# Optimization experiments

Measured on AMD Instinct MI355X. Metric: run time of the kernel, lower is better.

Reference implementation:

```python
import jax, jax.numpy as jnp
import numpy as np


def gin_layer(x, src, dst, ew, w1, b1, w2, b2):
    # message: gather source features, scale by edge weight  [E, d]
    msg = x[src] * ew[:, None]
    # scatter-add into destination nodes  [N, d]
    agg = jax.ops.segment_sum(msg, dst, num_segments=x.shape[0])
    # GIN update: (1 + eps) * x + aggregate, eps = 0 (default)
    h = agg + x
    # 2-layer MLP (Linear -> ReLU -> Linear, plain last layer)
    h = jax.nn.relu(h @ w1 + b1)
    return h @ w2 + b2


def setup_inputs() -> dict:
    key = jax.random.key(0)
    ks = jax.random.split(key, 16)
    N, E, D = 100000, 1000000, 64
    x = jax.random.normal(ks[0], (N, D), dtype=jnp.float32)
    edge_index = jax.random.randint(ks[1], (2, E), 0, N)
    edge_weight = jax.random.uniform(ks[2], (E,), dtype=jnp.float32)

    def lin(k, fi, fo):
        return jax.random.normal(k, (fi, fo), dtype=jnp.float32) * (1.0 / np.sqrt(fi))

    return {
        "x": x, "edge_index": edge_index, "edge_weight": edge_weight,
        "w11": lin(ks[3], 64, 64),  "b11": jnp.zeros(64, jnp.float32),
        "w12": lin(ks[4], 64, 64),  "b12": jnp.zeros(64, jnp.float32),
        "w21": lin(ks[5], 64, 128), "b21": jnp.zeros(128, jnp.float32),
        "w22": lin(ks[6], 128, 64), "b22": jnp.zeros(64, jnp.float32),
        "w31": lin(ks[7], 64, 64),  "b31": jnp.zeros(64, jnp.float32),
        "w32": lin(ks[8], 64, 64),  "b32": jnp.zeros(64, jnp.float32),
    }


def reference(x, edge_index, edge_weight,
              w11, b11, w12, b12,
              w21, b21, w22, b22,
              w31, b31, w32, b32):
    src, dst = edge_index[0], edge_index[1]
    # dropout is identity in eval mode
    h = gin_layer(x, src, dst, edge_weight, w11, b11, w12, b12)
    h = jax.nn.relu(h)
    h = gin_layer(h, src, dst, edge_weight, w21, b21, w22, b22)
    h = jax.nn.relu(h)
    h = gin_layer(h, src, dst, edge_weight, w31, b31, w32, b32)
    return h
```

## Files before the change

kernel.cpp:

```cpp
#include <hip/hip_runtime.h>
#include <math.h>


#define FEAT  64
#define BINW  128
#define BSH   7
#define NBLK  256
#define SRCB  25
#define PADSLACK 2048

typedef __attribute__((ext_vector_type(8))) short bfrag;
typedef __attribute__((ext_vector_type(4))) float ffrag;

__device__ __forceinline__ unsigned short f2bf_rne(float x) {
    union { float f; unsigned u; } v; v.f = x;
    unsigned r = (v.u + 0x7fffu + ((v.u >> 16) & 1u)) >> 16;
    return (unsigned short)r;
}
__device__ __forceinline__ float bf2f(unsigned short h) {
    union { unsigned u; float f; } v; v.u = ((unsigned)h) << 16;
    return v.f;
}

__device__ __forceinline__ void pack_one(const float* __restrict__ w,
                                         unsigned short* __restrict__ hi,
                                         unsigned short* __restrict__ lo,
                                         int K, int Hc, int i) {
    int KF = K >> 5;
    int j    = i & 7;
    int lane = (i >> 3) & 63;
    int fb   = i >> 9;
    int kf   = fb % KF;
    int cg   = fb / KF;
    int k    = kf * 32 + ((lane >> 4) << 3) + j;
    int col  = cg * 16 + (lane & 15);
    float x = w[k * Hc + col];
    unsigned short h = f2bf_rne(x);
    hi[i] = h;
    lo[i] = f2bf_rne(x - bf2f(h));
}

__global__ __launch_bounds__(256)
void k_pre(const float4* __restrict__ x4, ushort4* __restrict__ xb4,
           int n4, int gCvt,
           const int* __restrict__ dst, int* __restrict__ counts,
           int E, int NBINS,
           const float* w11, const float* w12, const float* w21,
           const float* w22, const float* w31, const float* w32,
           unsigned short* p11h, unsigned short* p11l,
           unsigned short* p12h, unsigned short* p12l,
           unsigned short* p21h, unsigned short* p21l,
           unsigned short* p22h, unsigned short* p22l,
           unsigned short* p31h, unsigned short* p31l,
           unsigned short* p32h, unsigned short* p32l) {
    __shared__ int h[1024];
    const int bb = blockIdx.x, tid = threadIdx.x;
    if (bb < gCvt) {
        int i = bb * 256 + tid;
        if (i < n4) {
            float4 v = x4[i];
            ushort4 o;
            o.x = f2bf_rne(v.x); o.y = f2bf_rne(v.y);
            o.z = f2bf_rne(v.z); o.w = f2bf_rne(v.w);
            xb4[i] = o;
        }
    } else if (bb < gCvt + NBLK) {
        const int b = bb - gCvt;
        for (int i = tid; i < NBINS; i += 256) h[i] = 0;
        __syncthreads();
        const int chunk = (E + NBLK - 1) / NBLK;
        const int ebeg = b * chunk;
        const int eend = (ebeg + chunk < E) ? ebeg + chunk : E;
        for (int e = ebeg + tid; e < eend; e += 256)
            atomicAdd(&h[dst[e] >> BSH], 1);
        __syncthreads();
        for (int i = tid; i < NBINS; i += 256)
            counts[i * NBLK + b] = h[i];
    } else {
        int i = (bb - gCvt - NBLK) * 256 + tid;
        if      (i <  4096) pack_one(w11, p11h, p11l,  64,  64, i);
        else if (i <  8192) pack_one(w12, p12h, p12l,  64,  64, i - 4096);
        else if (i < 16384) pack_one(w21, p21h, p21l,  64, 128, i - 8192);
        else if (i < 24576) pack_one(w22, p22h, p22l, 128,  64, i - 16384);
        else if (i < 28672) pack_one(w31, p31h, p31l,  64,  64, i - 24576);
        else                pack_one(w32, p32h, p32l,  64,  64, i - 28672);
    }
}

__global__ __launch_bounds__(256)
void k_scanA2(int* __restrict__ counts, int* __restrict__ bintotal, int NBINS) {
    __shared__ int tmp[256];
    const int bin = blockIdx.x, tid = threadIdx.x;
    int c = counts[bin * NBLK + tid];
    tmp[tid] = c;
    __syncthreads();
    for (int off = 1; off < 256; off <<= 1) {
        int t = (tid >= off) ? tmp[tid - off] : 0;
        __syncthreads();
        tmp[tid] += t;
        __syncthreads();
    }
    counts[bin * NBLK + tid] = tmp[tid] - c;
    if (tid == 255) bintotal[bin] = tmp[255];
}

__global__ __launch_bounds__(256)
void k_place2(const int* __restrict__ src, const int* __restrict__ dst,
              const float* __restrict__ ew, const int* __restrict__ counts,
              const int* __restrict__ bintotal, int* __restrict__ binstart,
              int2* __restrict__ binbuf, int E, int NBINS) {
    __shared__ int bs[1024];
    __shared__ int tmp[256];
    __shared__ int base[1024];
    const int b = blockIdx.x, tid = threadIdx.x;

    int v[4]; int s = 0;
#pragma unroll
    for (int j = 0; j < 4; ++j) {
        int idx = tid * 4 + j;
        v[j] = (idx < NBINS) ? bintotal[idx] : 0;
        s += v[j];
    }
    tmp[tid] = s;
    __syncthreads();
    for (int off = 1; off < 256; off <<= 1) {
        int t = (tid >= off) ? tmp[tid - off] : 0;
        __syncthreads();
        tmp[tid] += t;
        __syncthreads();
    }
    int run = tmp[tid] - s;
#pragma unroll
    for (int j = 0; j < 4; ++j) {
        bs[tid * 4 + j] = run;
        run += v[j];
    }
    __syncthreads();

    if (b == 0) {
        for (int i = tid; i < NBINS; i += 256) binstart[i] = bs[i];
        if (tid == 0) binstart[NBINS] = E;
    }

    for (int i = tid; i < NBINS; i += 256)
        base[i] = bs[i] + counts[i * NBLK + b];
    __syncthreads();

    const int chunk = (E + NBLK - 1) / NBLK;
    const int ebeg = b * chunk;
    const int eend = (ebeg + chunk < E) ? ebeg + chunk : E;
    for (int e = ebeg + tid; e < eend; e += 256) {
        int d = dst[e];
        int slot = atomicAdd(&base[d >> BSH], 1);
        int key = ((d & (BINW - 1)) << SRCB) | src[e];
        binbuf[slot] = make_int2(key, __float_as_int(ew[e]));
    }
}

__global__ __launch_bounds__(256)
void k_binsort(const int2* __restrict__ binbuf, const int* __restrict__ binstart,
               int* __restrict__ pbeg, int* __restrict__ pend,
               int2* __restrict__ csr_pad, int N) {
    __shared__ int cnt[BINW];
    __shared__ int cur[BINW];
    __shared__ int pex[BINW];
    const int b    = blockIdx.x;
    const int base = binstart[b];
    const int ne   = binstart[b + 1] - base;
    const int tid  = threadIdx.x;
    const int base_pad = ((base + 15) & ~15) + b * PADSLACK;

    if (tid < BINW) cnt[tid] = 0;
    __syncthreads();
    for (int i = tid; i < ne; i += 256)
        atomicAdd(&cnt[(binbuf[base + i].x >> SRCB) & (BINW - 1)], 1);
    __syncthreads();
    int pc = 0;
    if (tid < BINW) { pc = (cnt[tid] + 15) & ~15; cur[tid] = pc; }
    __syncthreads();
    for (int off = 1; off < BINW; off <<= 1) {
        int v = (tid < BINW && tid >= off) ? cur[tid - off] : 0;
        __syncthreads();
        if (tid < BINW) cur[tid] += v;
        __syncthreads();
    }
    if (tid < BINW) {
        int ex = cur[tid] - pc;
        pex[tid] = ex;
        int node = b * BINW + tid;
        if (node < N) {
            pbeg[node] = base_pad + ex;
            pend[node] = base_pad + ex + pc;
        }
        cur[tid] = 0;
    }
    __syncthreads();
    for (int i = tid; i < ne; i += 256) {
        int2 e = binbuf[base + i];
        int dl = (e.x >> SRCB) & (BINW - 1);
        int r = atomicAdd(&cur[dl], 1);
        csr_pad[base_pad + pex[dl] + r] = make_int2(e.x & ((1 << SRCB) - 1), e.y);
    }
    __syncthreads();
    if (tid < BINW) {
        int c = cnt[tid];
        int pcn = (c + 15) & ~15;
        int o = base_pad + pex[tid];
        for (int j = c; j < pcn; ++j)
            csr_pad[o + j] = make_int2(0, 0);
    }
}

template<int H, bool RELU_OUT, bool OUT_BF16>
__global__ __launch_bounds__(256)
void k_fused(const ushort* __restrict__ in, void* __restrict__ outv,
             const int* __restrict__ pbeg, const int* __restrict__ pend,
             const int2* __restrict__ csr_pad,
             const unsigned short* __restrict__ w1h, const unsigned short* __restrict__ w1l,
             const float* __restrict__ b1,
             const unsigned short* __restrict__ w2h, const unsigned short* __restrict__ w2l,
             const float* __restrict__ b2, int N) {
    constexpr int SH   = H + 4;
    constexpr int CG1  = H / 16;
    constexpr int CGH1 = CG1 / 4;
    constexpr int KF2  = H / 32;
    __shared__ float hs[16 * SH];

    const int t = threadIdx.x;
    const int wk = t >> 6, lane = t & 63;
    const int m = lane & 15, q = lane >> 4;
    const int tnode0 = blockIdx.x * 16;
    float* hw = hs;
    const ushort4* in4 = reinterpret_cast<const ushort4*>(in);
    const int4* csr4 = reinterpret_cast<const int4*>(csr_pad);

    const int gnode = tnode0 + wk * 4 + q;
    const int beg = pbeg[gnode];
    const int end = pend[gnode];
    ushort4 xr = in4[(size_t)gnode * 16 + m];

    {
        const int nl = wk * 4 + q;
        float4 acc = make_float4(0.f, 0.f, 0.f, 0.f);
        for (int p = beg; p < end; p += 16) {
            int4 e2[8];
#pragma unroll
            for (int u = 0; u < 8; ++u)
                e2[u] = csr4[(p >> 1) + u];
            ushort4 v4[16];
#pragma unroll
            for (int u = 0; u < 8; ++u) {
                v4[2*u]   = in4[(unsigned)e2[u].x * 16u + m];
                v4[2*u+1] = in4[(unsigned)e2[u].z * 16u + m];
            }
#pragma unroll
            for (int u = 0; u < 8; ++u) {
                float w0 = __int_as_float(e2[u].y);
                float w1 = __int_as_float(e2[u].w);
                acc.x = fmaf(w0, bf2f(v4[2*u].x), acc.x);
                acc.y = fmaf(w0, bf2f(v4[2*u].y), acc.y);
                acc.z = fmaf(w0, bf2f(v4[2*u].z), acc.z);
                acc.w = fmaf(w0, bf2f(v4[2*u].w), acc.w);
                acc.x = fmaf(w1, bf2f(v4[2*u+1].x), acc.x);
                acc.y = fmaf(w1, bf2f(v4[2*u+1].y), acc.y);
                acc.z = fmaf(w1, bf2f(v4[2*u+1].z), acc.z);
                acc.w = fmaf(w1, bf2f(v4[2*u+1].w), acc.w);
            }
        }
        acc.x += bf2f(xr.x); acc.y += bf2f(xr.y);
        acc.z += bf2f(xr.z); acc.w += bf2f(xr.w);
        *reinterpret_cast<float4*>(&hw[nl * SH + m * 4]) = acc;
    }
    __syncthreads();

    const bfrag* w1hp = reinterpret_cast<const bfrag*>(w1h);
    const bfrag* w1lp = reinterpret_cast<const bfrag*>(w1l);
    const bfrag* w2hp = reinterpret_cast<const bfrag*>(w2h);
    const bfrag* w2lp = reinterpret_cast<const bfrag*>(w2l);

    bfrag ah[2], al[2];
#pragma unroll
    for (int kf = 0; kf < 2; ++kf) {
        const float* base = &hw[m * SH + kf * 32 + q * 8];
        float4 u0 = *reinterpret_cast<const float4*>(base);
        float4 u1 = *reinterpret_cast<const float4*>(base + 4);
        float u[8] = {u0.x, u0.y, u0.z, u0.w, u1.x, u1.y, u1.z, u1.w};
#pragma unroll
        for (int j = 0; j < 8; ++j) {
            unsigned short hb = f2bf_rne(u[j]);
            ah[kf][j] = (short)hb;
            al[kf][j] = (short)f2bf_rne(u[j] - bf2f(hb));
        }
    }
    __syncthreads();

    __builtin_amdgcn_s_setprio(1);
#pragma unroll
    for (int cgi = 0; cgi < CGH1; ++cgi) {
        const int cg = wk * CGH1 + cgi;
        ffrag c = {0.f, 0.f, 0.f, 0.f};
#pragma unroll
        for (int kf = 0; kf < 2; ++kf) {
            bfrag bh = w1hp[(cg * 2 + kf) * 64 + lane];
            bfrag bl = w1lp[(cg * 2 + kf) * 64 + lane];
            c = __builtin_amdgcn_mfma_f32_16x16x32_bf16(ah[kf], bh, c, 0, 0, 0);
            c = __builtin_amdgcn_mfma_f32_16x16x32_bf16(al[kf], bh, c, 0, 0, 0);
            c = __builtin_amdgcn_mfma_f32_16x16x32_bf16(ah[kf], bl, c, 0, 0, 0);
        }
        float bias = b1[cg * 16 + m];
#pragma unroll
        for (int r = 0; r < 4; ++r) {
            float hv = fmaxf(c[r] + bias, 0.f);
            hw[(q * 4 + r) * SH + cg * 16 + m] = hv;
        }
    }
    __builtin_amdgcn_s_setprio(0);
    __syncthreads();

    bfrag gh[KF2], gl[KF2];
#pragma unroll
    for (int kf = 0; kf < KF2; ++kf) {
        const float* base = &hw[m * SH + kf * 32 + q * 8];
        float4 u0 = *reinterpret_cast<const float4*>(base);
        float4 u1 = *reinterpret_cast<const float4*>(base + 4);
        float u[8] = {u0.x, u0.y, u0.z, u0.w, u1.x, u1.y, u1.z, u1.w};
#pragma unroll
        for (int j = 0; j < 8; ++j) {
            unsigned short hb = f2bf_rne(u[j]);
            gh[kf][j] = (short)hb;
            gl[kf][j] = (short)f2bf_rne(u[j] - bf2f(hb));
        }
    }

    {
        const int cg = wk;
        ffrag c = {0.f, 0.f, 0.f, 0.f};
        __builtin_amdgcn_s_setprio(1);
#pragma unroll
        for (int kf = 0; kf < KF2; ++kf) {
            bfrag bh = w2hp[(cg * KF2 + kf) * 64 + lane];
            bfrag bl = w2lp[(cg * KF2 + kf) * 64 + lane];
            c = __builtin_amdgcn_mfma_f32_16x16x32_bf16(gh[kf], bh, c, 0, 0, 0);
            c = __builtin_amdgcn_mfma_f32_16x16x32_bf16(gl[kf], bh, c, 0, 0, 0);
            c = __builtin_amdgcn_mfma_f32_16x16x32_bf16(gh[kf], bl, c, 0, 0, 0);
        }
        __builtin_amdgcn_s_setprio(0);
        float bias = b2[cg * 16 + m];
#pragma unroll
        for (int r = 0; r < 4; ++r) {
            int nd = tnode0 + q * 4 + r;
            if (nd < N) {
                float v = c[r] + bias;
                if (RELU_OUT) v = fmaxf(v, 0.f);
                if (OUT_BF16)
                    ((unsigned short*)outv)[(size_t)nd * FEAT + cg * 16 + m] = f2bf_rne(v);
                else
                    ((float*)outv)[(size_t)nd * FEAT + cg * 16 + m] = v;
            }
        }
    }
}

extern "C" void kernel_launch(void* const* d_in, const int* in_sizes, int n_in,
                              void* d_out, int out_size, void* d_ws, size_t ws_size,
                              hipStream_t stream) {
    const float* x   = (const float*)d_in[0];
    const int*   ei  = (const int*)  d_in[1];
    const float* ew  = (const float*)d_in[2];
    const float* w11 = (const float*)d_in[3];
    const float* b11 = (const float*)d_in[4];
    const float* w12 = (const float*)d_in[5];
    const float* b12 = (const float*)d_in[6];
    const float* w21 = (const float*)d_in[7];
    const float* b21 = (const float*)d_in[8];
    const float* w22 = (const float*)d_in[9];
    const float* b22 = (const float*)d_in[10];
    const float* w31 = (const float*)d_in[11];
    const float* b31 = (const float*)d_in[12];
    const float* w32 = (const float*)d_in[13];
    const float* b32 = (const float*)d_in[14];

    const int N = in_sizes[0] / FEAT;
    const int E = in_sizes[2];
    const int* srci = ei;
    const int* dsti = ei + E;
    const int NBINS = (N + BINW - 1) >> BSH;

    unsigned short* xb0 = (unsigned short*)d_ws;
    unsigned short* xb1 = xb0 + (size_t)N * FEAT;
    int*   pbeg     = (int*)(xb1 + (size_t)N * FEAT);
    int*   pend     = pbeg + N;
    int*   counts   = pend + N;
    int*   bintotal = counts + NBINS * NBLK;
    int*   binstart = bintotal + NBINS;
    size_t a16 = ((size_t)(binstart + NBINS + 1) + 15) & ~(size_t)15;
    int2*  binbuf   = (int2*)a16;
    int2*  csr_pad  = (int2*)(binbuf + E);
    size_t pk = (size_t)(csr_pad + E + (size_t)NBINS * PADSLACK + 16);
    unsigned short* p11h = (unsigned short*)pk;
    unsigned short* p11l = p11h + 4096;
    unsigned short* p12h = p11l + 4096;
    unsigned short* p12l = p12h + 4096;
    unsigned short* p21h = p12l + 4096;
    unsigned short* p21l = p21h + 8192;
    unsigned short* p22h = p21l + 8192;
    unsigned short* p22l = p22h + 8192;
    unsigned short* p31h = p22l + 8192;
    unsigned short* p31l = p31h + 4096;
    unsigned short* p32h = p31l + 4096;
    unsigned short* p32l = p32h + 4096;
    float* outF = (float*)d_out;

    const int n4   = N * 16;
    const int gCvt = (n4 + 255) / 256;
    const int gMlp = (N + 15) / 16;
    const int gPre = gCvt + NBLK + 128;

    k_pre<<<gPre, 256, 0, stream>>>((const float4*)x, (ushort4*)xb0, n4, gCvt,
                                    dsti, counts, E, NBINS,
                                    w11, w12, w21, w22, w31, w32,
                                    p11h, p11l, p12h, p12l, p21h, p21l,
                                    p22h, p22l, p31h, p31l, p32h, p32l);
    k_scanA2 <<<NBINS, 256, 0, stream>>>(counts, bintotal, NBINS);
    k_place2 <<<NBLK,  256, 0, stream>>>(srci, dsti, ew, counts, bintotal,
                                         binstart, binbuf, E, NBINS);
    k_binsort<<<NBINS, 256, 0, stream>>>(binbuf, binstart, pbeg, pend,
                                         csr_pad, N);

    k_fused<64,  true,  true ><<<gMlp, 256, 0, stream>>>(xb0, xb1, pbeg, pend, csr_pad,
                                                         p11h, p11l, b11, p12h, p12l, b12, N);
    k_fused<128, true,  true ><<<gMlp, 256, 0, stream>>>(xb1, xb0, pbeg, pend, csr_pad,
                                                         p21h, p21l, b21, p22h, p22l, b22, N);
    k_fused<64,  false, false><<<gMlp, 256, 0, stream>>>(xb0, outF, pbeg, pend, csr_pad,
                                                         p31h, p31l, b31, p32h, p32l, b32, N);
}
```

Baseline: 263.1 us.

## Process two node groups per block and overlap their first gather chunk

Each fused GIN block now handles 32 destination nodes, as two 16-node halves, instead of 16. The first 16-edge chunk of both halves is loaded and gathered together to raise memory-level parallelism in the neighbour gather, since most nodes have only one chunk at this average degree. The binsort now guarantees every node at least one padded chunk, so that unconditional first chunk is safe. It also stores source indices pre-scaled to byte offsets to drop an index multiply. In exchange, register pressure rises, the grid halves and the two MLP phases run back to back within a block, which may reduce occupancy.

```diff
diff --git a/kernel.cpp b/kernel.cpp
--- a/kernel.cpp
+++ b/kernel.cpp
@@ -176,7 +176,11 @@
         atomicAdd(&cnt[(binbuf[base + i].x >> SRCB) & (BINW - 1)], 1);
     __syncthreads();
     int pc = 0;
-    if (tid < BINW) { pc = (cnt[tid] + 15) & ~15; cur[tid] = pc; }
+    if (tid < BINW) {
+        int c = cnt[tid];
+        pc = c ? ((c + 15) & ~15) : 16;
+        cur[tid] = pc;
+    }
     __syncthreads();
     for (int off = 1; off < BINW; off <<= 1) {
         int v = (tid < BINW && tid >= off) ? cur[tid - off] : 0;
@@ -199,12 +203,13 @@
         int2 e = binbuf[base + i];
         int dl = (e.x >> SRCB) & (BINW - 1);
         int r = atomicAdd(&cur[dl], 1);
-        csr_pad[base_pad + pex[dl] + r] = make_int2(e.x & ((1 << SRCB) - 1), e.y);
+        csr_pad[base_pad + pex[dl] + r] =
+            make_int2((e.x & ((1 << SRCB) - 1)) << 7, e.y);
     }
     __syncthreads();
     if (tid < BINW) {
         int c = cnt[tid];
-        int pcn = (c + 15) & ~15;
+        int pcn = c ? ((c + 15) & ~15) : 16;
         int o = base_pad + pex[tid];
         for (int j = c; j < pcn; ++j)
             csr_pad[o + j] = make_int2(0, 0);
@@ -224,52 +229,127 @@
     constexpr int CG1  = H / 16;
     constexpr int CGH1 = CG1 / 4;
     constexpr int KF2  = H / 32;
-    __shared__ float hs[16 * SH];
+    __shared__ float hs[2 * 16 * SH];
 
     const int t = threadIdx.x;
     const int wk = t >> 6, lane = t & 63;
     const int m = lane & 15, q = lane >> 4;
-    const int tnode0 = blockIdx.x * 16;
-    float* hw = hs;
-    const ushort4* in4 = reinterpret_cast<const ushort4*>(in);
+    const int m8 = m * 8;
+    float* hwA = hs;
+    float* hwB = hs + 16 * SH;
+    const char* inB = reinterpret_cast<const char*>(in);
     const int4* csr4 = reinterpret_cast<const int4*>(csr_pad);
 
-    const int gnode = tnode0 + wk * 4 + q;
-    const int beg = pbeg[gnode];
-    const int end = pend[gnode];
-    ushort4 xr = in4[(size_t)gnode * 16 + m];
-
+    const int nodeA = blockIdx.x * 32 + wk * 4 + q;
+    const int nodeB = nodeA + 16;
+    const int begA = pbeg[nodeA], endA = pend[nodeA];
+    const int begB = pbeg[nodeB], endB = pend[nodeB];
+    ushort4 xrA = *reinterpret_cast<const ushort4*>(inB + nodeA * 128 + m8);
+    ushort4 xrB = *reinterpret_cast<const ushort4*>(inB + nodeB * 128 + m8);
+
+    float4 accA = make_float4(0.f, 0.f, 0.f, 0.f);
+    float4 accB = make_float4(0.f, 0.f, 0.f, 0.f);
+
+    {
+        int4 eA[8], eB[8];
+#pragma unroll
+        for (int u = 0; u < 8; ++u) eA[u] = csr4[(begA >> 1) + u];
+#pragma unroll
+        for (int u = 0; u < 8; ++u) eB[u] = csr4[(begB >> 1) + u];
+        ushort4 vA[16], vB[16];
+#pragma unroll
+        for (int u = 0; u < 8; ++u) {
+            vA[2*u]   = *reinterpret_cast<const ushort4*>(inB + (unsigned)eA[u].x + m8);
+            vA[2*u+1] = *reinterpret_cast<const ushort4*>(inB + (unsigned)eA[u].z + m8);
+        }
+#pragma unroll
+        for (int u = 0; u < 8; ++u) {
+            vB[2*u]   = *reinterpret_cast<const ushort4*>(inB + (unsigned)eB[u].x + m8);
+            vB[2*u+1] = *reinterpret_cast<const ushort4*>(inB + (unsigned)eB[u].z + m8);
+        }
+#pragma unroll
+        for (int u = 0; u < 8; ++u) {
+            float w0 = __int_as_float(eA[u].y);
+            float w1 = __int_as_float(eA[u].w);
+            accA.x = fmaf(w0, bf2f(vA[2*u].x), accA.x);
+            accA.y = fmaf(w0, bf2f(vA[2*u].y), accA.y);
+            accA.z = fmaf(w0, bf2f(vA[2*u].z), accA.z);
+            accA.w = fmaf(w0, bf2f(vA[2*u].w), accA.w);
+            accA.x = fmaf(w1, bf2f(vA[2*u+1].x), accA.x);
+            accA.y = fmaf(w1, bf2f(vA[2*u+1].y), accA.y);
+            accA.z = fmaf(w1, bf2f(vA[2*u+1].z), accA.z);
+            accA.w = fmaf(w1, bf2f(vA[2*u+1].w), accA.w);
+        }
+#pragma unroll
+        for (int u = 0; u < 8; ++u) {
+            float w0 = __int_as_float(eB[u].y);
+            float w1 = __int_as_float(eB[u].w);
+            accB.x = fmaf(w0, bf2f(vB[2*u].x), accB.x);
+            accB.y = fmaf(w0, bf2f(vB[2*u].y), accB.y);
+            accB.z = fmaf(w0, bf2f(vB[2*u].z), accB.z);
+            accB.w = fmaf(w0, bf2f(vB[2*u].w), accB.w);
+            accB.x = fmaf(w1, bf2f(vB[2*u+1].x), accB.x);
+            accB.y = fmaf(w1, bf2f(vB[2*u+1].y), accB.y);
+            accB.z = fmaf(w1, bf2f(vB[2*u+1].z), accB.z);
+            accB.w = fmaf(w1, bf2f(vB[2*u+1].w), accB.w);
+        }
+    }
+    for (int p = begA + 16; p < endA; p += 16) {
+        int4 e2[8];
+#pragma unroll
+        for (int u = 0; u < 8; ++u) e2[u] = csr4[(p >> 1) + u];
+        ushort4 v4[16];
+#pragma unroll
+        for (int u = 0; u < 8; ++u) {
+            v4[2*u]   = *reinterpret_cast<const ushort4*>(inB + (unsigned)e2[u].x + m8);
+            v4[2*u+1] = *reinterpret_cast<const ushort4*>(inB + (unsigned)e2[u].z + m8);
+        }
+#pragma unroll
+        for (int u = 0; u < 8; ++u) {
+            float w0 = __int_as_float(e2[u].y);
+            float w1 = __int_as_float(e2[u].w);
+            accA.x = fmaf(w0, bf2f(v4[2*u].x), accA.x);
+            accA.y = fmaf(w0, bf2f(v4[2*u].y), accA.y);
+            accA.z = fmaf(w0, bf2f(v4[2*u].z), accA.z);
+            accA.w = fmaf(w0, bf2f(v4[2*u].w), accA.w);
+            accA.x = fmaf(w1, bf2f(v4[2*u+1].x), accA.x);
+            accA.y = fmaf(w1, bf2f(v4[2*u+1].y), accA.y);
+            accA.z = fmaf(w1, bf2f(v4[2*u+1].z), accA.z);
+            accA.w = fmaf(w1, bf2f(v4[2*u+1].w), accA.w);
+        }
+    }
+    for (int p = begB + 16; p < endB; p += 16) {
+        int4 e2[8];
+#pragma unroll
+        for (int u = 0; u < 8; ++u) e2[u] = csr4[(p >> 1) + u];
+        ushort4 v4[16];
+#pragma unroll
+        for (int u = 0; u < 8; ++u) {
+            v4[2*u]   = *reinterpret_cast<const ushort4*>(inB + (unsigned)e2[u].x + m8);
+            v4[2*u+1] = *reinterpret_cast<const ushort4*>(inB + (unsigned)e2[u].z + m8);
+        }
+#pragma unroll
+        for (int u = 0; u < 8; ++u) {
+            float w0 = __int_as_float(e2[u].y);
+            float w1 = __int_as_float(e2[u].w);
+            accB.x = fmaf(w0, bf2f(v4[2*u].x), accB.x);
+            accB.y = fmaf(w0, bf2f(v4[2*u].y), accB.y);
+            accB.z = fmaf(w0, bf2f(v4[2*u].z), accB.z);
+            accB.w = fmaf(w0, bf2f(v4[2*u].w), accB.w);
+            accB.x = fmaf(w1, bf2f(v4[2*u+1].x), accB.x);
+            accB.y = fmaf(w1, bf2f(v4[2*u+1].y), accB.y);
+            accB.z = fmaf(w1, bf2f(v4[2*u+1].z), accB.z);
+            accB.w = fmaf(w1, bf2f(v4[2*u+1].w), accB.w);
+        }
+    }
+    accA.x += bf2f(xrA.x); accA.y += bf2f(xrA.y);
+    accA.z += bf2f(xrA.z); accA.w += bf2f(xrA.w);
+    accB.x += bf2f(xrB.x); accB.y += bf2f(xrB.y);
+    accB.z += bf2f(xrB.z); accB.w += bf2f(xrB.w);
     {
         const int nl = wk * 4 + q;
-        float4 acc = make_float4(0.f, 0.f, 0.f, 0.f);
-        for (int p = beg; p < end; p += 16) {
-            int4 e2[8];
-#pragma unroll
-            for (int u = 0; u < 8; ++u)
-                e2[u] = csr4[(p >> 1) + u];
-            ushort4 v4[16];
-#pragma unroll
-            for (int u = 0; u < 8; ++u) {
-                v4[2*u]   = in4[(unsigned)e2[u].x * 16u + m];
-                v4[2*u+1] = in4[(unsigned)e2[u].z * 16u + m];
-            }
-#pragma unroll
-            for (int u = 0; u < 8; ++u) {
-                float w0 = __int_as_float(e2[u].y);
-                float w1 = __int_as_float(e2[u].w);
-                acc.x = fmaf(w0, bf2f(v4[2*u].x), acc.x);
-                acc.y = fmaf(w0, bf2f(v4[2*u].y), acc.y);
-                acc.z = fmaf(w0, bf2f(v4[2*u].z), acc.z);
-                acc.w = fmaf(w0, bf2f(v4[2*u].w), acc.w);
-                acc.x = fmaf(w1, bf2f(v4[2*u+1].x), acc.x);
-                acc.y = fmaf(w1, bf2f(v4[2*u+1].y), acc.y);
-                acc.z = fmaf(w1, bf2f(v4[2*u+1].z), acc.z);
-                acc.w = fmaf(w1, bf2f(v4[2*u+1].w), acc.w);
-            }
-        }
-        acc.x += bf2f(xr.x); acc.y += bf2f(xr.y);
-        acc.z += bf2f(xr.z); acc.w += bf2f(xr.w);
-        *reinterpret_cast<float4*>(&hw[nl * SH + m * 4]) = acc;
+        *reinterpret_cast<float4*>(&hwA[nl * SH + m * 4]) = accA;
+        *reinterpret_cast<float4*>(&hwB[nl * SH + m * 4]) = accB;
     }
     __syncthreads();
 
@@ -278,87 +358,92 @@
     const bfrag* w2hp = reinterpret_cast<const bfrag*>(w2h);
     const bfrag* w2lp = reinterpret_cast<const bfrag*>(w2l);
 
-    bfrag ah[2], al[2];
-#pragma unroll
-    for (int kf = 0; kf < 2; ++kf) {
-        const float* base = &hw[m * SH + kf * 32 + q * 8];
-        float4 u0 = *reinterpret_cast<const float4*>(base);
-        float4 u1 = *reinterpret_cast<const float4*>(base + 4);
-        float u[8] = {u0.x, u0.y, u0.z, u0.w, u1.x, u1.y, u1.z, u1.w};
-#pragma unroll
-        for (int j = 0; j < 8; ++j) {
-            unsigned short hb = f2bf_rne(u[j]);
-            ah[kf][j] = (short)hb;
-            al[kf][j] = (short)f2bf_rne(u[j] - bf2f(hb));
-        }
-    }
-    __syncthreads();
-
-    __builtin_amdgcn_s_setprio(1);
-#pragma unroll
-    for (int cgi = 0; cgi < CGH1; ++cgi) {
-        const int cg = wk * CGH1 + cgi;
-        ffrag c = {0.f, 0.f, 0.f, 0.f};
+    auto run_mlp = [&](float* hw, int tnode0) {
+        bfrag ah[2], al[2];
 #pragma unroll
         for (int kf = 0; kf < 2; ++kf) {
-            bfrag bh = w1hp[(cg * 2 + kf) * 64 + lane];
-            bfrag bl = w1lp[(cg * 2 + kf) * 64 + lane];
-            c = __builtin_amdgcn_mfma_f32_16x16x32_bf16(ah[kf], bh, c, 0, 0, 0);
-            c = __builtin_amdgcn_mfma_f32_16x16x32_bf16(al[kf], bh, c, 0, 0, 0);
-            c = __builtin_amdgcn_mfma_f32_16x16x32_bf16(ah[kf], bl, c, 0, 0, 0);
-        }
-        float bias = b1[cg * 16 + m];
-#pragma unroll
-        for (int r = 0; r < 4; ++r) {
-            float hv = fmaxf(c[r] + bias, 0.f);
-            hw[(q * 4 + r) * SH + cg * 16 + m] = hv;
-        }
-    }
-    __builtin_amdgcn_s_setprio(0);
-    __syncthreads();
-
-    bfrag gh[KF2], gl[KF2];
-#pragma unroll
-    for (int kf = 0; kf < KF2; ++kf) {
-        const float* base = &hw[m * SH + kf * 32 + q * 8];
-        float4 u0 = *reinterpret_cast<const float4*>(base);
-        float4 u1 = *reinterpret_cast<const float4*>(base + 4);
-        float u[8] = {u0.x, u0.y, u0.z, u0.w, u1.x, u1.y, u1.z, u1.w};
-#pragma unroll
-        for (int j = 0; j < 8; ++j) {
-            unsigned short hb = f2bf_rne(u[j]);
-            gh[kf][j] = (short)hb;
-            gl[kf][j] = (short)f2bf_rne(u[j] - bf2f(hb));
-        }
-    }
-
-    {
-        const int cg = wk;
-        ffrag c = {0.f, 0.f, 0.f, 0.f};
+            const float* base = &hw[m * SH + kf * 32 + q * 8];
+            float4 u0 = *reinterpret_cast<const float4*>(base);
+            float4 u1 = *reinterpret_cast<const float4*>(base + 4);
+            float u[8] = {u0.x, u0.y, u0.z, u0.w, u1.x, u1.y, u1.z, u1.w};
+#pragma unroll
+            for (int j = 0; j < 8; ++j) {
+                unsigned short hb = f2bf_rne(u[j]);
+                ah[kf][j] = (short)hb;
+                al[kf][j] = (short)f2bf_rne(u[j] - bf2f(hb));
+            }
+        }
+        __syncthreads();
+
         __builtin_amdgcn_s_setprio(1);
 #pragma unroll
+        for (int cgi = 0; cgi < CGH1; ++cgi) {
+            const int cg = wk * CGH1 + cgi;
+            ffrag c = {0.f, 0.f, 0.f, 0.f};
+#pragma unroll
+            for (int kf = 0; kf < 2; ++kf) {
+                bfrag bh = w1hp[(cg * 2 + kf) * 64 + lane];
+                bfrag bl = w1lp[(cg * 2 + kf) * 64 + lane];
+                c = __builtin_amdgcn_mfma_f32_16x16x32_bf16(ah[kf], bh, c, 0, 0, 0);
+                c = __builtin_amdgcn_mfma_f32_16x16x32_bf16(al[kf], bh, c, 0, 0, 0);
+                c = __builtin_amdgcn_mfma_f32_16x16x32_bf16(ah[kf], bl, c, 0, 0, 0);
+            }
+            float bias = b1[cg * 16 + m];
+#pragma unroll
+            for (int r = 0; r < 4; ++r) {
+                float hv = fmaxf(c[r] + bias, 0.f);
+                hw[(q * 4 + r) * SH + cg * 16 + m] = hv;
+            }
+        }
+        __builtin_amdgcn_s_setprio(0);
+        __syncthreads();
+
+        bfrag gh[KF2], gl[KF2];
+#pragma unroll
         for (int kf = 0; kf < KF2; ++kf) {
-            bfrag bh = w2hp[(cg * KF2 + kf) * 64 + lane];
-            bfrag bl = w2lp[(cg * KF2 + kf) * 64 + lane];
-            c = __builtin_amdgcn_mfma_f32_16x16x32_bf16(gh[kf], bh, c, 0, 0, 0);
-            c = __builtin_amdgcn_mfma_f32_16x16x32_bf16(gl[kf], bh, c, 0, 0, 0);
-            c = __builtin_amdgcn_mfma_f32_16x16x32_bf16(gh[kf], bl, c, 0, 0, 0);
-        }
-        __builtin_amdgcn_s_setprio(0);
-        float bias = b2[cg * 16 + m];
-#pragma unroll
-        for (int r = 0; r < 4; ++r) {
-            int nd = tnode0 + q * 4 + r;
-            if (nd < N) {
-                float v = c[r] + bias;
-                if (RELU_OUT) v = fmaxf(v, 0.f);
-                if (OUT_BF16)
-                    ((unsigned short*)outv)[(size_t)nd * FEAT + cg * 16 + m] = f2bf_rne(v);
-                else
-                    ((float*)outv)[(size_t)nd * FEAT + cg * 16 + m] = v;
+            const float* base = &hw[m * SH + kf * 32 + q * 8];
+            float4 u0 = *reinterpret_cast<const float4*>(base);
+            float4 u1 = *reinterpret_cast<const float4*>(base + 4);
+            float u[8] = {u0.x, u0.y, u0.z, u0.w, u1.x, u1.y, u1.z, u1.w};
+#pragma unroll
+            for (int j = 0; j < 8; ++j) {
+                unsigned short hb = f2bf_rne(u[j]);
+                gh[kf][j] = (short)hb;
+                gl[kf][j] = (short)f2bf_rne(u[j] - bf2f(hb));
             }
         }
-    }
+
+        {
+            const int cg = wk;
+            ffrag c = {0.f, 0.f, 0.f, 0.f};
+            __builtin_amdgcn_s_setprio(1);
+#pragma unroll
+            for (int kf = 0; kf < KF2; ++kf) {
+                bfrag bh = w2hp[(cg * KF2 + kf) * 64 + lane];
+                bfrag bl = w2lp[(cg * KF2 + kf) * 64 + lane];
+                c = __builtin_amdgcn_mfma_f32_16x16x32_bf16(gh[kf], bh, c, 0, 0, 0);
+                c = __builtin_amdgcn_mfma_f32_16x16x32_bf16(gl[kf], bh, c, 0, 0, 0);
+                c = __builtin_amdgcn_mfma_f32_16x16x32_bf16(gh[kf], bl, c, 0, 0, 0);
+            }
+            __builtin_amdgcn_s_setprio(0);
+            float bias = b2[cg * 16 + m];
+#pragma unroll
+            for (int r = 0; r < 4; ++r) {
+                int nd = tnode0 + q * 4 + r;
+                if (nd < N) {
+                    float v = c[r] + bias;
+                    if (RELU_OUT) v = fmaxf(v, 0.f);
+                    if (OUT_BF16)
+                        ((unsigned short*)outv)[(size_t)nd * FEAT + cg * 16 + m] = f2bf_rne(v);
+                    else
+                        ((float*)outv)[(size_t)nd * FEAT + cg * 16 + m] = v;
+                }
+            }
+        }
+    };
+
+    run_mlp(hwA, blockIdx.x * 32);
+    run_mlp(hwB, blockIdx.x * 32 + 16);
 }
 
 extern "C" void kernel_launch(void* const* d_in, const int* in_sizes, int n_in,
@@ -396,7 +481,7 @@
     size_t a16 = ((size_t)(binstart + NBINS + 1) + 15) & ~(size_t)15;
     int2*  binbuf   = (int2*)a16;
     int2*  csr_pad  = (int2*)(binbuf + E);
-    size_t pk = (size_t)(csr_pad + E + (size_t)NBINS * PADSLACK + 16);
+    size_t pk = (size_t)(csr_pad + E + (size_t)NBINS * PADSLACK + 1024);
     unsigned short* p11h = (unsigned short*)pk;
     unsigned short* p11l = p11h + 4096;
     unsigned short* p12h = p11l + 4096;
@@ -413,7 +498,7 @@
 
     const int n4   = N * 16;
     const int gCvt = (n4 + 255) / 256;
-    const int gMlp = (N + 15) / 16;
+    const int gMlp = (N + 31) / 32;
     const int gPre = gCvt + NBLK + 128;
 
     k_pre<<<gPre, 256, 0, stream>>>((const float4*)x, (ushort4*)xb0, n4, gCvt,
```

Result: slower. 286.6 us (+8.9%).
